# Kernel tuning notes

Hardware: AMD Instinct MI355X
Metric: run time of the kernel (lower is better)

Reference implementation:

```python
import jax, jax.numpy as jnp
import numpy as np

NUM_HEADS = 32
NUM_KV_HEADS = 8
HEAD_DIM = 128
SCALING = 0.08838834764831845  # 1/sqrt(128)
B, T = 2, 2048


def setup_inputs() -> dict:
    key = jax.random.key(0)
    kq, kk, kv = jax.random.split(key, 3)
    q = jax.random.normal(kq, (B, T, NUM_HEADS, HEAD_DIM), dtype=jnp.float32)
    k = jax.random.normal(kk, (B, T, NUM_KV_HEADS, HEAD_DIM), dtype=jnp.float32)
    v = jax.random.normal(kv, (B, T, NUM_KV_HEADS, HEAD_DIM), dtype=jnp.float32)
    return {"q": q, "k": k, "v": v}


def _attn(q, k, v):
    # GQA expand: [B,T,nKv,D] -> [B,T,nH,D]
    n_rep = NUM_HEADS // NUM_KV_HEADS
    Bq, Tq = q.shape[0], q.shape[1]
    k = jnp.broadcast_to(k[:, :, :, None, :], (Bq, Tq, NUM_KV_HEADS, n_rep, HEAD_DIM)).reshape(Bq, Tq, NUM_HEADS, HEAD_DIM)
    v = jnp.broadcast_to(v[:, :, :, None, :], (Bq, Tq, NUM_KV_HEADS, n_rep, HEAD_DIM)).reshape(Bq, Tq, NUM_HEADS, HEAD_DIM)
    # scores: [B,H,T,T]
    scores = jnp.einsum('bqhd,bkhd->bhqk', q, k) * SCALING
    causal = jnp.triu(jnp.ones((Tq, Tq), dtype=bool), k=1)  # True above diagonal
    scores = jnp.where(causal, jnp.finfo(scores.dtype).min, scores)
    probs = jax.nn.softmax(scores, axis=-1)
    out = jnp.einsum('bhqk,bkhd->bqhd', probs, v)
    return out.reshape(Bq, Tq, NUM_HEADS * HEAD_DIM)


def reference(q, k, v):
    return _attn(q, k, v)
```

## Files before the change

### kernel.cpp

```cpp
#include <hip/hip_runtime.h>
#include <stdint.h>


typedef __attribute__((ext_vector_type(8))) __bf16 bf16x8;
typedef __attribute__((ext_vector_type(16))) float f32x16;

#define QSCALE (0.08838834764831845f * 1.4426950408889634f)

__global__ __launch_bounds__(256) void cvt_k(const float* __restrict__ k,
                                             unsigned short* __restrict__ kb) {
    unsigned tid = blockIdx.x * 256u + threadIdx.x;
    unsigned s = tid & 15u;
    unsigned h = (tid >> 4) & 7u;
    unsigned t = (tid >> 7) & 2047u;
    unsigned b = tid >> 18;
    const float4* src = (const float4*)(k + (size_t)tid * 8u);
    float4 f0 = src[0], f1 = src[1];
    bf16x8 r;
    r[0] = (__bf16)f0.x; r[1] = (__bf16)f0.y; r[2] = (__bf16)f0.z; r[3] = (__bf16)f0.w;
    r[4] = (__bf16)f1.x; r[5] = (__bf16)f1.y; r[6] = (__bf16)f1.z; r[7] = (__bf16)f1.w;
    size_t o = ((size_t)((b * 8u + h) * 2048u + t) * 16u + (s ^ (t & 7u))) * 8u;
    *(bf16x8*)(kb + o) = r;
}

__global__ __launch_bounds__(256) void cvt_v(const float* __restrict__ v,
                                             unsigned short* __restrict__ vtb) {
    unsigned tid = blockIdx.x * 256u + threadIdx.x;
    unsigned d = tid & 127u;
    unsigned oct = (tid >> 7) & 3u;
    unsigned tile = (tid >> 9) & 63u;
    unsigned kvh = (tid >> 15) & 7u;
    unsigned b = tid >> 18;
    const float* src = v + ((size_t)(b * 2048u + tile * 32u + oct * 8u) * 8u + kvh) * 128u + d;
    bf16x8 r;
#pragma unroll
    for (int e = 0; e < 8; ++e) r[e] = (__bf16)src[(size_t)e * 1024u];
    unsigned p = d >> 1;
    unsigned slot = (d & 1u) * 4u + oct;
    size_t off = (size_t)(b * 8u + kvh) * 262144u + (size_t)tile * 4096u
               + (p * 8u + (slot ^ (p & 7u))) * 8u;
    *(bf16x8*)(vtb + off) = r;
}

__device__ inline void load16_lds(const void* g, void* l) {
    __builtin_amdgcn_global_load_lds(
        (__attribute__((address_space(1))) void*)(g),
        (__attribute__((address_space(3))) void*)(l), 16, 0, 0);
}

union BW2 { unsigned u; __bf16 h[2]; };
union BW8 { unsigned u[4]; bf16x8 v; };

__global__ __launch_bounds__(256, 3) void attn_fwd(const float* __restrict__ qg,
                                                   const unsigned short* __restrict__ kb,
                                                   const unsigned short* __restrict__ vtb,
                                                   float* __restrict__ outg) {
    __shared__ __align__(16) unsigned short K0[32*128], K1[32*128], K2[32*128], K3[32*128];
    __shared__ __align__(16) unsigned short V0[64*64],  V1[64*64],  V2[64*64],  V3[64*64];

    int bid = blockIdx.x;
    int kvh = bid & 7;
    int pos = bid >> 3;
    int qt = 15 - (pos >> 3);
    int sub = pos & 7;
    int b = sub & 1;
    int h = kvh * 4 + (sub >> 1);

    int tid = threadIdx.x;
    int lane = tid & 63;
    int lq = lane & 31;
    int hi = lane >> 5;
    bool bhi = (hi != 0);
    int q0w = qt * 128 + (tid >> 6) * 32;
    int nt = 4 * (qt + 1);

    const unsigned short* kT = kb + (size_t)(b * 8 + kvh) * 262144u;
    const unsigned short* vT = vtb + (size_t)(b * 8 + kvh) * 262144u;

    auto stage = [&](int t, unsigned short* kd, unsigned short* vd) {
        const char* ks = (const char*)(kT + (size_t)t * 4096u);
        const char* vs = (const char*)(vT + (size_t)t * 4096u);
#pragma unroll
        for (int i = 0; i < 2; ++i) {
            load16_lds(ks + (i * 256 + tid) * 16, kd + (i * 256 + tid) * 8);
            load16_lds(vs + (i * 256 + tid) * 16, vd + (i * 256 + tid) * 8);
        }
    };

    stage(0, K0, V0);
    stage(1, K1, V1);

    bf16x8 qf[8];
    {
        const float* qp = qg + ((size_t)(b * 2048 + q0w + lq) * 32u + h) * 128u;
#pragma unroll
        for (int c = 0; c < 8; ++c) {
            int d0 = c * 16 + hi * 8;
            float4 f0 = *(const float4*)(qp + d0);
            float4 f1 = *(const float4*)(qp + d0 + 4);
            qf[c][0] = (__bf16)(f0.x * QSCALE); qf[c][1] = (__bf16)(f0.y * QSCALE);
            qf[c][2] = (__bf16)(f0.z * QSCALE); qf[c][3] = (__bf16)(f0.w * QSCALE);
            qf[c][4] = (__bf16)(f1.x * QSCALE); qf[c][5] = (__bf16)(f1.y * QSCALE);
            qf[c][6] = (__bf16)(f1.z * QSCALE); qf[c][7] = (__bf16)(f1.w * QSCALE);
        }
    }

    f32x16 acc[4];
#pragma unroll
    for (int dt = 0; dt < 4; ++dt)
#pragma unroll
        for (int r = 0; r < 16; ++r) acc[dt][r] = 0.f;
    float lrun = 0.f;
    f32x16 stA, stB;

#define ITER(T, CUR, PRV, KC, VP, KS, VS)                                        \
    do {                                                                          \
        int t_ = (T);                                                             \
        if (t_ + 2 < nt) { asm volatile("s_waitcnt vmcnt(4)" ::: "memory"); }     \
        else             { asm volatile("s_waitcnt vmcnt(0)" ::: "memory"); }     \
        __builtin_amdgcn_s_barrier();                                             \
        if (t_ + 2 < nt) stage(t_ + 2, KS, VS);                                   \
        int kv0_ = t_ * 32;                                                       \
        if (kv0_ <= q0w + 31) {                                 \
            _Pragma("unroll")                                                     \
            for (int r = 0; r < 16; ++r) CUR[r] = 0.f;                            \
            __builtin_amdgcn_s_setprio(1);                                        \
            _Pragma("unroll")                                                     \
            for (int c = 0; c < 8; ++c) {                                         \
                bf16x8 kf = *(const bf16x8*)&KC[lq * 128 +                        \
                                (((2 * c + hi) ^ (lq & 7)) << 3)];                \
                CUR = __builtin_amdgcn_mfma_f32_32x32x16_bf16(kf, qf[c], CUR,     \
                                                              0, 0, 0);           \
            }                                                                     \
            __builtin_amdgcn_s_setprio(0);                                        \
            if (kv0_ == q0w) {                                 \
                _Pragma("unroll")                                                 \
                for (int r = 0; r < 16; ++r) {                                    \
                    int kvl = (r & 3) + 8 * (r >> 2) + 4 * hi;                    \
                    if (kvl > lq) CUR[r] = -1e30f;                                \
                }                                                                 \
            }                                                                     \
        }                                                                         \
        if (t_ >= 1 && kv0_ - 32 <= q0w + 31) {              \
            _Pragma("unroll")                                                     \
            for (int r = 0; r < 16; ++r) PRV[r] = exp2f(PRV[r]);                  \
            unsigned wv[8];                                                       \
            _Pragma("unroll")                                                     \
            for (int i = 0; i < 8; ++i) {                                         \
                BW2 t2; t2.h[0] = (__bf16)PRV[2*i]; t2.h[1] = (__bf16)PRV[2*i+1]; \
                wv[i] = t2.u;                                                     \
            }                                                                     \
            unsigned u0 = bhi ? wv[0] : wv[2]; u0 = __shfl_xor(u0, 32);           \
            unsigned u1 = bhi ? wv[1] : wv[3]; u1 = __shfl_xor(u1, 32);           \
            unsigned u2 = bhi ? wv[4] : wv[6]; u2 = __shfl_xor(u2, 32);           \
            unsigned u3 = bhi ? wv[5] : wv[7]; u3 = __shfl_xor(u3, 32);           \
            BW8 pb0, pb1;                                                         \
            pb0.u[0] = bhi ? u0 : wv[0]; pb0.u[1] = bhi ? u1 : wv[1];             \
            pb0.u[2] = bhi ? wv[2] : u0; pb0.u[3] = bhi ? wv[3] : u1;             \
            pb1.u[0] = bhi ? u2 : wv[4]; pb1.u[1] = bhi ? u3 : wv[5];             \
            pb1.u[2] = bhi ? wv[6] : u2; pb1.u[3] = bhi ? wv[7] : u3;             \
            __builtin_amdgcn_s_setprio(1);                                        \
            _Pragma("unroll")                                                     \
            for (int dt = 0; dt < 4; ++dt) {                                      \
                int drow = dt * 32 + lq;                                          \
                int pp = drow >> 1;                                               \
                int s0 = (drow & 1) * 4 + hi;                                     \
                bf16x8 vf0 = *(const bf16x8*)&VP[pp * 64 + ((s0 ^ (pp & 7)) << 3)];\
                acc[dt] = __builtin_amdgcn_mfma_f32_32x32x16_bf16(vf0, pb0.v,     \
                                                                  acc[dt], 0,0,0);\
                bf16x8 vf1 = *(const bf16x8*)&VP[pp * 64 +                        \
                                               (((s0 + 2) ^ (pp & 7)) << 3)];     \
                acc[dt] = __builtin_amdgcn_mfma_f32_32x32x16_bf16(vf1, pb1.v,     \
                                                                  acc[dt], 0,0,0);\
            }                                                                     \
            __builtin_amdgcn_s_setprio(0);                                        \
            float s8[8];                                                          \
            _Pragma("unroll")                                                     \
            for (int i = 0; i < 8; ++i) s8[i] = PRV[2*i] + PRV[2*i+1];            \
            _Pragma("unroll")                                                     \
            for (int i = 0; i < 4; ++i) s8[i] = s8[i] + s8[i + 4];                \
            lrun += (s8[0] + s8[1]) + (s8[2] + s8[3]);                            \
        }                                                                         \
    } while (0)

    for (int t = 0; t < nt; t += 4) {
        ITER(t + 0, stA, stB, K0, V3, K2, V2);
        ITER(t + 1, stB, stA, K1, V0, K3, V3);
        ITER(t + 2, stA, stB, K2, V1, K0, V0);
        ITER(t + 3, stB, stA, K3, V2, K1, V1);
    }
    ITER(nt, stA, stB, K0, V3, K0, V0);
#undef ITER

    lrun += __shfl_xor(lrun, 32);
    float il = 1.0f / lrun;
    float* ob = outg + ((size_t)(b * 2048 + q0w + lq) * 32u + h) * 128u;
#pragma unroll
    for (int dt = 0; dt < 4; ++dt)
#pragma unroll
        for (int rq = 0; rq < 4; ++rq) {
            int d = dt * 32 + rq * 8 + hi * 4;
            float4 o4 = { acc[dt][rq * 4 + 0] * il, acc[dt][rq * 4 + 1] * il,
                          acc[dt][rq * 4 + 2] * il, acc[dt][rq * 4 + 3] * il };
            *(float4*)(ob + d) = o4;
        }
}

extern "C" void kernel_launch(void* const* d_in, const int* in_sizes, int n_in,
                              void* d_out, int out_size, void* d_ws, size_t ws_size,
                              hipStream_t stream) {
    const float* q = (const float*)d_in[0];
    const float* k = (const float*)d_in[1];
    const float* v = (const float*)d_in[2];
    float* out = (float*)d_out;
    unsigned short* kbuf = (unsigned short*)d_ws;
    unsigned short* vbuf = kbuf + (size_t)2 * 8 * 2048 * 128;
    cvt_k<<<2048, 256, 0, stream>>>(k, kbuf);
    cvt_v<<<2048, 256, 0, stream>>>(v, vbuf);
    attn_fwd<<<1024, 256, 0, stream>>>(q, kbuf, vbuf, out);
}
```

Measured before the change: 134.6 us.

## Permute K rows so QK^T output feeds PV MFMA directly, drop shuffles

K rows are permuted within each 32-row tile at conversion time so that the QK^T MFMA accumulator layout lines up with the B-operand layout the PV MFMA expects. This removes the cross-half-wave shuffles and selects that repacked the probabilities, and the causal mask is adjusted for the permuted key order. The software pipeline that overlapped tile t's QK^T with tile t-1's PV is removed, and the LDS ring shrinks from four to three K/V buffers. Less LDS could allow higher occupancy, but losing the QK/PV overlap may expose MFMA and exp latency.

After: 133.8 us. About the same (-0.7%).

```diff
diff --git a/kernel.cpp b/kernel.cpp
--- a/kernel.cpp
+++ b/kernel.cpp
@@ -6,6 +6,11 @@
 typedef __attribute__((ext_vector_type(16))) float f32x16;
 
 #define QSCALE (0.08838834764831845f * 1.4426950408889634f)
+
+__host__ __device__ inline unsigned pi32(unsigned x) {
+    unsigned q2 = (x >> 2) & 3u;
+    return (q2 == 1u || q2 == 2u) ? (x ^ 12u) : x;
+}
 
 __global__ __launch_bounds__(256) void cvt_k(const float* __restrict__ k,
                                              unsigned short* __restrict__ kb) {
@@ -19,7 +24,8 @@
     bf16x8 r;
     r[0] = (__bf16)f0.x; r[1] = (__bf16)f0.y; r[2] = (__bf16)f0.z; r[3] = (__bf16)f0.w;
     r[4] = (__bf16)f1.x; r[5] = (__bf16)f1.y; r[6] = (__bf16)f1.z; r[7] = (__bf16)f1.w;
-    size_t o = ((size_t)((b * 8u + h) * 2048u + t) * 16u + (s ^ (t & 7u))) * 8u;
+    unsigned tp = (t & ~31u) | pi32(t & 31u);
+    size_t o = ((size_t)((b * 8u + h) * 2048u + tp) * 16u + (s ^ (tp & 7u))) * 8u;
     *(bf16x8*)(kb + o) = r;
 }
 
@@ -55,8 +61,8 @@
                                                    const unsigned short* __restrict__ kb,
                                                    const unsigned short* __restrict__ vtb,
                                                    float* __restrict__ outg) {
-    __shared__ __align__(16) unsigned short K0[32*128], K1[32*128], K2[32*128], K3[32*128];
-    __shared__ __align__(16) unsigned short V0[64*64],  V1[64*64],  V2[64*64],  V3[64*64];
+    __shared__ __align__(16) unsigned short K0[32 * 128], K1[32 * 128], K2[32 * 128];
+    __shared__ __align__(16) unsigned short V0[64 * 64],  V1[64 * 64],  V2[64 * 64];
 
     int bid = blockIdx.x;
     int kvh = bid & 7;
@@ -70,7 +76,6 @@
     int lane = tid & 63;
     int lq = lane & 31;
     int hi = lane >> 5;
-    bool bhi = (hi != 0);
     int q0w = qt * 128 + (tid >> 6) * 32;
     int nt = 4 * (qt + 1);
 
@@ -105,70 +110,75 @@
         }
     }
 
+    float zz;
+    asm volatile("v_mov_b32 %0, 0" : "=v"(zz));
+    f32x16 z16;
+#pragma unroll
+    for (int r = 0; r < 16; ++r) z16[r] = zz;
+
     f32x16 acc[4];
 #pragma unroll
     for (int dt = 0; dt < 4; ++dt)
 #pragma unroll
         for (int r = 0; r < 16; ++r) acc[dt][r] = 0.f;
     float lrun = 0.f;
-    f32x16 stA, stB;
-
-#define ITER(T, CUR, PRV, KC, VP, KS, VS)                                        \
+
+#define ITER(TB, KC, VC, KS, VS)                                                  \
     do {                                                                          \
-        int t_ = (T);                                                             \
-        if (t_ + 2 < nt) { asm volatile("s_waitcnt vmcnt(4)" ::: "memory"); }     \
-        else             { asm volatile("s_waitcnt vmcnt(0)" ::: "memory"); }     \
-        __builtin_amdgcn_s_barrier();                                             \
-        if (t_ + 2 < nt) stage(t_ + 2, KS, VS);                                   \
-        int kv0_ = t_ * 32;                                                       \
-        if (kv0_ <= q0w + 31) {                                 \
-            _Pragma("unroll")                                                     \
-            for (int r = 0; r < 16; ++r) CUR[r] = 0.f;                            \
+        int tb_ = (TB);                                                           \
+        if (tb_ + 2 < nt) {                                                       \
+            asm volatile("s_waitcnt vmcnt(4)" ::: "memory");                      \
+            __builtin_amdgcn_s_barrier();                                         \
+            stage(tb_ + 2, KS, VS);                                               \
+        } else {                                                                  \
+            asm volatile("s_waitcnt vmcnt(0)" ::: "memory");                      \
+            __builtin_amdgcn_s_barrier();                                         \
+        }                                                                         \
+        int kv0_ = tb_ * 32;                                                      \
+        if (kv0_ <= q0w + 31) {                            \
+            f32x16 st0;                                                           \
             __builtin_amdgcn_s_setprio(1);                                        \
-            _Pragma("unroll")                                                     \
-            for (int c = 0; c < 8; ++c) {                                         \
+            {                                                                     \
+                bf16x8 kf = *(const bf16x8*)&KC[lq * 128 + ((hi ^ (lq & 7)) << 3)];\
+                st0 = __builtin_amdgcn_mfma_f32_32x32x16_bf16(kf, qf[0], z16,     \
+                                                              0, 0, 0);           \
+            }                                                                     \
+            _Pragma("unroll")                                                     \
+            for (int c = 1; c < 8; ++c) {                                         \
                 bf16x8 kf = *(const bf16x8*)&KC[lq * 128 +                        \
                                 (((2 * c + hi) ^ (lq & 7)) << 3)];                \
-                CUR = __builtin_amdgcn_mfma_f32_32x32x16_bf16(kf, qf[c], CUR,     \
+                st0 = __builtin_amdgcn_mfma_f32_32x32x16_bf16(kf, qf[c], st0,     \
                                                               0, 0, 0);           \
             }                                                                     \
             __builtin_amdgcn_s_setprio(0);                                        \
-            if (kv0_ == q0w) {                                 \
+            if (kv0_ == q0w) {                       \
                 _Pragma("unroll")                                                 \
                 for (int r = 0; r < 16; ++r) {                                    \
                     int kvl = (r & 3) + 8 * (r >> 2) + 4 * hi;                    \
-                    if (kvl > lq) CUR[r] = -1e30f;                                \
+                    int q2 = (kvl >> 2) & 3;                                      \
+                    int kva = (q2 == 1 || q2 == 2) ? (kvl ^ 12) : kvl;            \
+                    if (kva > lq) st0[r] = -1e30f;                                \
                 }                                                                 \
             }                                                                     \
-        }                                                                         \
-        if (t_ >= 1 && kv0_ - 32 <= q0w + 31) {              \
-            _Pragma("unroll")                                                     \
-            for (int r = 0; r < 16; ++r) PRV[r] = exp2f(PRV[r]);                  \
-            unsigned wv[8];                                                       \
-            _Pragma("unroll")                                                     \
-            for (int i = 0; i < 8; ++i) {                                         \
-                BW2 t2; t2.h[0] = (__bf16)PRV[2*i]; t2.h[1] = (__bf16)PRV[2*i+1]; \
-                wv[i] = t2.u;                                                     \
-            }                                                                     \
-            unsigned u0 = bhi ? wv[0] : wv[2]; u0 = __shfl_xor(u0, 32);           \
-            unsigned u1 = bhi ? wv[1] : wv[3]; u1 = __shfl_xor(u1, 32);           \
-            unsigned u2 = bhi ? wv[4] : wv[6]; u2 = __shfl_xor(u2, 32);           \
-            unsigned u3 = bhi ? wv[5] : wv[7]; u3 = __shfl_xor(u3, 32);           \
+            _Pragma("unroll")                                                     \
+            for (int r = 0; r < 16; ++r) st0[r] = exp2f(st0[r]);                  \
             BW8 pb0, pb1;                                                         \
-            pb0.u[0] = bhi ? u0 : wv[0]; pb0.u[1] = bhi ? u1 : wv[1];             \
-            pb0.u[2] = bhi ? wv[2] : u0; pb0.u[3] = bhi ? wv[3] : u1;             \
-            pb1.u[0] = bhi ? u2 : wv[4]; pb1.u[1] = bhi ? u3 : wv[5];             \
-            pb1.u[2] = bhi ? wv[6] : u2; pb1.u[3] = bhi ? wv[7] : u3;             \
+            _Pragma("unroll")                                                     \
+            for (int i = 0; i < 4; ++i) {                                         \
+                BW2 a; a.h[0] = (__bf16)st0[2 * i];     a.h[1] = (__bf16)st0[2 * i + 1]; \
+                BW2 c; c.h[0] = (__bf16)st0[8 + 2 * i]; c.h[1] = (__bf16)st0[9 + 2 * i]; \
+                pb0.u[i] = a.u; pb1.u[i] = c.u;                                   \
+            }                                                                     \
             __builtin_amdgcn_s_setprio(1);                                        \
             _Pragma("unroll")                                                     \
             for (int dt = 0; dt < 4; ++dt) {                                      \
                 int drow = dt * 32 + lq;                                          \
                 int pp = drow >> 1;                                               \
                 int s0 = (drow & 1) * 4 + hi;                                     \
-                bf16x8 vf0 = *(const bf16x8*)&VP[pp * 64 + ((s0 ^ (pp & 7)) << 3)];\
+                bf16x8 vf0 = *(const bf16x8*)&VC[pp * 64 + ((s0 ^ (pp & 7)) << 3)];\
                 acc[dt] = __builtin_amdgcn_mfma_f32_32x32x16_bf16(vf0, pb0.v,     \
                                                                   acc[dt], 0,0,0);\
-                bf16x8 vf1 = *(const bf16x8*)&VP[pp * 64 +                        \
+                bf16x8 vf1 = *(const bf16x8*)&VC[pp * 64 +                        \
                                                (((s0 + 2) ^ (pp & 7)) << 3)];     \
                 acc[dt] = __builtin_amdgcn_mfma_f32_32x32x16_bf16(vf1, pb1.v,     \
                                                                   acc[dt], 0,0,0);\
@@ -176,20 +186,18 @@
             __builtin_amdgcn_s_setprio(0);                                        \
             float s8[8];                                                          \
             _Pragma("unroll")                                                     \
-            for (int i = 0; i < 8; ++i) s8[i] = PRV[2*i] + PRV[2*i+1];            \
+            for (int i = 0; i < 8; ++i) s8[i] = st0[2 * i] + st0[2 * i + 1];      \
             _Pragma("unroll")                                                     \
             for (int i = 0; i < 4; ++i) s8[i] = s8[i] + s8[i + 4];                \
             lrun += (s8[0] + s8[1]) + (s8[2] + s8[3]);                            \
         }                                                                         \
     } while (0)
 
-    for (int t = 0; t < nt; t += 4) {
-        ITER(t + 0, stA, stB, K0, V3, K2, V2);
-        ITER(t + 1, stB, stA, K1, V0, K3, V3);
-        ITER(t + 2, stA, stB, K2, V1, K0, V0);
-        ITER(t + 3, stB, stA, K3, V2, K1, V1);
+    for (int t = 0; t < nt; t += 3) {
+        ITER(t + 0, K0, V0, K2, V2);
+        if (t + 1 < nt) ITER(t + 1, K1, V1, K0, V0);
+        if (t + 2 < nt) ITER(t + 2, K2, V2, K1, V1);
     }
-    ITER(nt, stA, stB, K0, V3, K0, V0);
 #undef ITER
 
     lrun += __shfl_xor(lrun, 32);
```
